# Optimization experiments

Hardware: AMD Instinct MI355X
Metric: run time of the kernel (lower is better)

Reference implementation:

```python
import jax, jax.numpy as jnp
import numpy as np

N = 100000
C_IN = 128
HEADS = 4
D_HEAD = 32
E = 1600000
NEG_SLOPE = 0.2
LN_EPS = 1e-5


def setup_inputs() -> dict:
    key = jax.random.key(0)
    ks = jax.random.split(key, 8)
    x = jax.random.normal(ks[0], (N, C_IN), dtype=jnp.float32)
    edge_index = jax.random.randint(ks[1], (2, E), 0, N, dtype=jnp.int32)
    # LayerNorm affine params
    ln_gamma = jnp.ones((C_IN,), jnp.float32)
    ln_beta = jnp.zeros((C_IN,), jnp.float32)
    # GATv2 linear layers (lin_l for source/messages, lin_r for target), glorot-ish scale
    scale = 1.0 / np.sqrt(C_IN)
    W_l = jax.random.normal(ks[2], (C_IN, HEADS * D_HEAD), jnp.float32) * scale
    b_l = jnp.zeros((HEADS * D_HEAD,), jnp.float32)
    W_r = jax.random.normal(ks[3], (C_IN, HEADS * D_HEAD), jnp.float32) * scale
    b_r = jnp.zeros((HEADS * D_HEAD,), jnp.float32)
    att = jax.random.normal(ks[4], (HEADS, D_HEAD), jnp.float32) * (1.0 / np.sqrt(D_HEAD))
    bias = jnp.zeros((D_HEAD,), jnp.float32)  # concat=False -> out_channels bias
    return {"x": x, "edge_index": edge_index, "ln_gamma": ln_gamma, "ln_beta": ln_beta,
            "W_l": W_l, "b_l": b_l, "W_r": W_r, "b_r": b_r, "att": att, "bias": bias}


def reference(x, edge_index, ln_gamma, ln_beta, W_l, b_l, W_r, b_r, att, bias):
    n = x.shape[0]
    # LayerNorm + ReLU (dropout_mask=None / eval mode)
    mu = jnp.mean(x, axis=-1, keepdims=True)
    var = jnp.mean(jnp.square(x - mu), axis=-1, keepdims=True)
    xh = (x - mu) * jax.lax.rsqrt(var + LN_EPS) * ln_gamma + ln_beta
    xh = jax.nn.relu(xh)
    # add self loops
    loops = jnp.arange(n, dtype=edge_index.dtype)
    src = jnp.concatenate([edge_index[0], loops])  # message sources j
    dst = jnp.concatenate([edge_index[1], loops])  # aggregation targets i
    # GATv2: separate transforms for source and target
    x_l = (xh @ W_l + b_l).reshape(n, HEADS, D_HEAD)
    x_r = (xh @ W_r + b_r).reshape(n, HEADS, D_HEAD)
    # edge scores: e_ij = att . leaky_relu(x_l[j] + x_r[i])
    s = x_l[src] + x_r[dst]                                      # [E+N, H, Dh]
    e = jnp.einsum('ehd,hd->eh', jax.nn.leaky_relu(s, NEG_SLOPE), att)
    # segment softmax over destination node
    m = jax.ops.segment_max(e, dst, num_segments=n)              # [N, H]
    w = jnp.exp(e - m[dst])
    denom = jax.ops.segment_sum(w, dst, num_segments=n)          # [N, H]
    alpha = w / (denom[dst] + 1e-16)                             # [E+N, H]
    # scatter-aggregate messages alpha * x_l[j]
    out = jax.ops.segment_sum(alpha[:, :, None] * x_l[src], dst, num_segments=n)  # [N, H, Dh]
    # concat=False -> mean over heads, then bias
    return out.mean(axis=1) + bias
```

## Files before the change

kernel.cpp:

```cpp
#include <hip/hip_runtime.h>
#include <math.h>


typedef __bf16 bf16x8 __attribute__((ext_vector_type(8)));
typedef float f32x4 __attribute__((ext_vector_type(4)));
typedef _Float16 h2 __attribute__((ext_vector_type(2)));

#define BIN_T 4096
#define NB_MAX 1024
#define AST 136
#define HST 136

static __device__ __forceinline__ unsigned short f2bf(float f) {
  union { float f; unsigned u; } v;
  v.f = f;
  const unsigned r = v.u + 0x7fffu + ((v.u >> 16) & 1u);
  return (unsigned short)(r >> 16);
}
static __device__ __forceinline__ float bf2f(unsigned short h) {
  union { float f; unsigned u; } v;
  v.u = ((unsigned)h) << 16;
  return v.f;
}

static __device__ __forceinline__ float quad_reduce_add(float p) {
  int a = __builtin_amdgcn_mov_dpp(__builtin_bit_cast(int, p),
                                   0xB1 , 0xf, 0xf,
                                   true);
  p += __builtin_bit_cast(float, a);
  int b = __builtin_amdgcn_mov_dpp(__builtin_bit_cast(int, p),
                                   0x4E , 0xf, 0xf,
                                   true);
  p += __builtin_bit_cast(float, b);
  return p;
}

__global__ __launch_bounds__(256) void hist_pack_k(
    const int* __restrict__ dst_arr, int* __restrict__ bucket_cnt,
    const float* __restrict__ Wl, const float* __restrict__ Wr,
    unsigned short* __restrict__ wph, unsigned short* __restrict__ wpl,
    int E, int NB) {
  __shared__ int h[NB_MAX];
  const int t = threadIdx.x;
  const int gtid = blockIdx.x * 256 + t;
  for (int b = t; b < NB; b += 256) h[b] = 0;
  if (gtid < 32768) {
    const int mat = gtid >> 14;
    const int rem = gtid & 16383;
    const int k = rem >> 7;
    const int c = rem & 127;
    const float v = (mat ? Wr : Wl)[rem];
    const unsigned short hh = f2bf(v);
    const unsigned short lo = f2bf(v - bf2f(hh));
    const int po = ((mat * 4 + (k >> 5)) * 128 + c) * 32 + (k & 31);
    wph[po] = hh;
    wpl[po] = lo;
  }
  __syncthreads();
  const int beg = blockIdx.x * BIN_T;
  const int end = min(beg + BIN_T, E);
  for (int j0 = beg + t * 4; j0 < end; j0 += 1024) {
    if (j0 + 4 <= end) {
      const int4 d4 = *(const int4*)(dst_arr + j0);
      atomicAdd(&h[d4.x >> 7], 1);
      atomicAdd(&h[d4.y >> 7], 1);
      atomicAdd(&h[d4.z >> 7], 1);
      atomicAdd(&h[d4.w >> 7], 1);
    } else {
      for (int j = j0; j < end; j++) atomicAdd(&h[dst_arr[j] >> 7], 1);
    }
  }
  __syncthreads();
  for (int b = t; b < NB; b += 256) {
    const int v = h[b];
    if (v) atomicAdd(&bucket_cnt[b], v);
  }
}

__global__ __launch_bounds__(1024) void bucket_scan_k(
    const int* __restrict__ bucket_cnt, int* __restrict__ bucket_edge_off,
    int* __restrict__ bucket_cur, int* __restrict__ offsets,
    int NB, int N, int M) {
  __shared__ int lds[1024];
  const int t = threadIdx.x;
  const int v = (t < NB) ? bucket_cnt[t] : 0;
  lds[t] = v;
  __syncthreads();
  for (int d = 1; d < 1024; d <<= 1) {
    int u = 0;
    if (t >= d) u = lds[t - d];
    __syncthreads();
    lds[t] += u;
    __syncthreads();
  }
  if (t < NB) {
    const int excl = lds[t] - v;
    bucket_edge_off[t] = excl;
    bucket_cur[t] = excl;
    if (t == NB - 1) bucket_edge_off[NB] = lds[t];
  }
  if (t == 0) offsets[N] = M;
}

__global__ __launch_bounds__(512, 5) void gemm_bin_fat_k(
    const float* __restrict__ x, const float* __restrict__ gamma,
    const float* __restrict__ beta,
    const unsigned short* __restrict__ wph,
    const unsigned short* __restrict__ wpl,
    const float* __restrict__ bl, const float* __restrict__ br,
    _Float16* __restrict__ xl16, _Float16* __restrict__ xr16,
    const int* __restrict__ ei, int* __restrict__ bucket_cur,
    unsigned* __restrict__ binned,
    int n, int E, int NB, int nchunks) {
  __shared__ char smem[64 * AST * 2 * 2];
  const int t = threadIdx.x;

  if ((int)blockIdx.x < nchunks) {
    int* const h = (int*)smem;
    int* const cur = h + NB_MAX;
    for (int b = t; b < NB; b += 512) h[b] = 0;
    __syncthreads();
    const int beg = blockIdx.x * BIN_T;
    const int end = min(beg + BIN_T, E);
    for (int j0 = beg + t * 4; j0 < end; j0 += 2048) {
      if (j0 + 4 <= end) {
        const int4 d4 = *(const int4*)(ei + E + j0);
        atomicAdd(&h[d4.x >> 7], 1);
        atomicAdd(&h[d4.y >> 7], 1);
        atomicAdd(&h[d4.z >> 7], 1);
        atomicAdd(&h[d4.w >> 7], 1);
      } else {
        for (int j = j0; j < end; j++) atomicAdd(&h[ei[E + j] >> 7], 1);
      }
    }
    __syncthreads();
    for (int b = t; b < NB; b += 512) {
      const int v = h[b];
      cur[b] = v ? atomicAdd(&bucket_cur[b], v) : 0;
    }
    __syncthreads();
    for (int j0 = beg + t * 4; j0 < end; j0 += 2048) {
      if (j0 + 4 <= end) {
        const int4 s4 = *(const int4*)(ei + j0);
        const int4 d4 = *(const int4*)(ei + E + j0);
        binned[atomicAdd(&cur[d4.x >> 7], 1)] =
            (((unsigned)d4.x & 127u) << 25) | (unsigned)s4.x;
        binned[atomicAdd(&cur[d4.y >> 7], 1)] =
            (((unsigned)d4.y & 127u) << 25) | (unsigned)s4.y;
        binned[atomicAdd(&cur[d4.z >> 7], 1)] =
            (((unsigned)d4.z & 127u) << 25) | (unsigned)s4.z;
        binned[atomicAdd(&cur[d4.w >> 7], 1)] =
            (((unsigned)d4.w & 127u) << 25) | (unsigned)s4.w;
      } else {
        for (int j = j0; j < end; j++) {
          const int s = ei[j], d = ei[E + j];
          binned[atomicAdd(&cur[d >> 7], 1)] =
              (((unsigned)d & 127u) << 25) | (unsigned)s;
        }
      }
    }
    return;
  }

  unsigned short* const ah = (unsigned short*)smem;
  unsigned short* const al = ah + 64 * AST;
  _Float16* const sth = (_Float16*)smem;
  const int blk = (blockIdx.x - nchunks) * 64;

  {
    const int r = t >> 3, q = t & 7;
    const int node = blk + r;
    float4 v[4];
    float s = 0.f, s2 = 0.f;
    const float* xrow = x + (size_t)node * 128;
#pragma unroll
    for (int rep = 0; rep < 4; rep++) {
      float4 f = make_float4(0.f, 0.f, 0.f, 0.f);
      if (node < n) f = *(const float4*)(xrow + 4 * q + 32 * rep);
      v[rep] = f;
      s += f.x + f.y + f.z + f.w;
      s2 += f.x * f.x + f.y * f.y + f.z * f.z + f.w * f.w;
    }
    s += __shfl_xor(s, 1);  s += __shfl_xor(s, 2);  s += __shfl_xor(s, 4);
    s2 += __shfl_xor(s2, 1); s2 += __shfl_xor(s2, 2); s2 += __shfl_xor(s2, 4);
    const float mu = s * (1.f / 128.f);
    const float rs = rsqrtf(s2 * (1.f / 128.f) - mu * mu + 1e-5f);
#pragma unroll
    for (int rep = 0; rep < 4; rep++) {
      const int k0 = 4 * q + 32 * rep;
      const float4 g4 = *(const float4*)(gamma + k0);
      const float4 b4 = *(const float4*)(beta + k0);
      const float ev[4] = {v[rep].x, v[rep].y, v[rep].z, v[rep].w};
      const float gv[4] = {g4.x, g4.y, g4.z, g4.w};
      const float bv[4] = {b4.x, b4.y, b4.z, b4.w};
      unsigned short hs[4], ls[4];
#pragma unroll
      for (int i2 = 0; i2 < 4; i2++) {
        float xv = (ev[i2] - mu) * rs * gv[i2] + bv[i2];
        xv = fmaxf(xv, 0.f);
        const unsigned short h = f2bf(xv);
        hs[i2] = h;
        ls[i2] = f2bf(xv - bf2f(h));
      }
      *(ushort4*)(&ah[r * AST + k0]) = make_ushort4(hs[0], hs[1], hs[2], hs[3]);
      *(ushort4*)(&al[r * AST + k0]) = make_ushort4(ls[0], ls[1], ls[2], ls[3]);
    }
  }
  __syncthreads();

  const int lane = t & 63;
  const int w = t >> 6;
  const int mat = w >> 2;
  const int cbase = (w & 3) * 32;
  const int m16 = lane & 15;
  const int quad = lane >> 4;
  const float* const biasp = mat ? br : bl;

  f32x4 acc[2][4];
  float bc[2];
#pragma unroll
  for (int ct = 0; ct < 2; ct++) {
    const int c = cbase + ct * 16 + m16;
    bf16x8 Bh[4], Bl8[4];
#pragma unroll
    for (int kb = 0; kb < 4; kb++) {
      const int bo = ((mat * 4 + kb) * 128 + c) * 32 + quad * 8;
      Bh[kb]  = *(const bf16x8*)(wph + bo);
      Bl8[kb] = *(const bf16x8*)(wpl + bo);
    }
    bc[ct] = biasp[c];
#pragma unroll
    for (int rt = 0; rt < 4; rt++) {
      f32x4 a = {0.f, 0.f, 0.f, 0.f};
#pragma unroll
      for (int kb = 0; kb < 4; kb++) {
        const int ao = (rt * 16 + m16) * AST + kb * 32 + quad * 8;
        const bf16x8 Ah  = *(const bf16x8*)(ah + ao);
        const bf16x8 Al8 = *(const bf16x8*)(al + ao);
        a = __builtin_amdgcn_mfma_f32_16x16x32_bf16(Ah,  Bh[kb],  a, 0, 0, 0);
        a = __builtin_amdgcn_mfma_f32_16x16x32_bf16(Al8, Bh[kb],  a, 0, 0, 0);
        a = __builtin_amdgcn_mfma_f32_16x16x32_bf16(Ah,  Bl8[kb], a, 0, 0, 0);
      }
      acc[ct][rt] = a;
    }
  }

  unsigned short* const outs[2] = {(unsigned short*)xl16,
                                   (unsigned short*)xr16};
#pragma unroll
  for (int round = 0; round < 2; round++) {
    __syncthreads();
    if (mat == 1 - round) {
#pragma unroll
      for (int ct = 0; ct < 2; ct++)
#pragma unroll
        for (int rt = 0; rt < 4; rt++)
#pragma unroll
          for (int g = 0; g < 4; g++)
            sth[(rt * 16 + quad * 4 + g) * HST + cbase + ct * 16 + m16] =
                (_Float16)(acc[ct][rt][g] + bc[ct]);
    }
    __syncthreads();
    unsigned short* const dst = outs[1 - round];
#pragma unroll
    for (int pass = 0; pass < 2; pass++) {
      const int idx = pass * 512 + t;
      const int row = idx >> 4;
      const int c8 = (idx & 15) * 8;
      const int node = blk + row;
      if (node < n)
        *(uint4*)(dst + (size_t)node * 128 + c8) =
            *(const uint4*)((const unsigned short*)sth + row * HST + c8);
    }
  }
}

__global__ __launch_bounds__(512) void csr_build_k(
    const unsigned* __restrict__ binned,
    const int* __restrict__ bucket_edge_off,
    unsigned* __restrict__ csr_src, int* __restrict__ offsets, int N, int M) {
  __shared__ int s_cnt[128];
  __shared__ int s_off[128];
  __shared__ int s_cur[128];
  const int b = blockIdx.x;
  const int t = threadIdx.x;
  if (b == 0 && t < 16) csr_src[M + t] = 0;
  const int eb = bucket_edge_off[b];
  const int ee = bucket_edge_off[b + 1];
  const int node0 = b << 7;
  if (t < 128) s_cnt[t] = 0;
  __syncthreads();
  for (int j = eb + t; j < ee; j += 512) {
    atomicAdd(&s_cnt[binned[j] >> 25], 1);
  }
  __syncthreads();
  int w = 0;
  if (t < 128) w = (node0 + t < N) ? (s_cnt[t] + 1) : 0;
  if (t < 128) s_off[t] = w;
  __syncthreads();
  for (int d = 1; d < 128; d <<= 1) {
    int u = 0;
    if (t < 128 && t >= d) u = s_off[t - d];
    __syncthreads();
    if (t < 128) s_off[t] += u;
    __syncthreads();
  }
  const int base = eb + node0;
  if (t < 128) {
    const int excl = s_off[t] - w;
    const int node = node0 + t;
    if (node < N) {
      offsets[node] = base + excl;
      csr_src[base + excl] = (unsigned)node << 8;
      s_cur[t] = excl + 1;
    }
  }
  __syncthreads();
  for (int j = eb + t; j < ee; j += 512) {
    const unsigned e = binned[j];
    const int pos = atomicAdd(&s_cur[e >> 25], 1);
    csr_src[base + pos] = (e & 0x1ffffffu) << 8;
  }
}

__global__ __launch_bounds__(256) void agg_fused_k(
    const uint4* __restrict__ xl4, const uint4* __restrict__ xr4,
    const float* __restrict__ att, const unsigned* __restrict__ csr_src,
    const int* __restrict__ offsets, const float* __restrict__ bias,
    float* __restrict__ out, int n) {
  const int t = threadIdx.x;
  const int wid = t >> 6;
  const int lane = t & 63;
  const int u = lane & 15;
  const int g = lane >> 4;
  const int nwaves = gridDim.x * 4;

  h2 at[4];
  {
    const float L2E = 1.44269504f;
    const float4 a0 = *(const float4*)(att + u * 8);
    const float4 a1 = *(const float4*)(att + u * 8 + 4);
    at[0] = h2{(_Float16)(a0.x * L2E), (_Float16)(a0.y * L2E)};
    at[1] = h2{(_Float16)(a0.z * L2E), (_Float16)(a0.w * L2E)};
    at[2] = h2{(_Float16)(a1.x * L2E), (_Float16)(a1.y * L2E)};
    at[3] = h2{(_Float16)(a1.z * L2E), (_Float16)(a1.w * L2E)};
  }
  float4 b0, b1;
  if (lane < 4) {
    b0 = *(const float4*)(bias + lane * 8);
    b1 = *(const float4*)(bias + lane * 8 + 4);
  }

  const h2 slope = h2{(_Float16)0.2f, (_Float16)0.2f};
  const char* const xbu = (const char*)xl4 + ((unsigned)u << 4);
  union U { uint4 u4; h2 h[4]; unsigned ui[4]; };

  int i = blockIdx.x * 4 + wid;
  if (i >= n) return;

  int off = offsets[i];
  int end = offsets[i + 1];
  U xru; xru.u4 = xr4[(size_t)i * 16 + u];
  uint4 rA = *(const uint4*)(xbu + csr_src[off + g]);
  uint4 rB = *(const uint4*)(xbu + csr_src[off + 4 + g]);

  while (true) {
    const int inext = i + nwaves;
    const int isel = (inext < n) ? inext : i;
    const int offn = offsets[isel];
    const int endn = offsets[isel + 1];
    U xrn; xrn.u4 = xr4[(size_t)isel * 16 + u];

    float den = 0.f;
    float acc[8] = {0.f, 0.f, 0.f, 0.f, 0.f, 0.f, 0.f, 0.f};

    for (int jb = off; jb < end; jb += 4) {
      U xv; xv.u4 = rA;
      rA = rB;
      rB = *(const uint4*)(xbu + csr_src[jb + 8 + g]);

      float p = 0.f;
#pragma unroll
      for (int k = 0; k < 4; k++) {
        const h2 s = xv.h[k] + xru.h[k];
        const h2 l = __builtin_elementwise_max(s, s * slope);
        p = __builtin_amdgcn_fdot2(l, at[k], p, false);
      }
      p = quad_reduce_add(p);

      const float wgt = (jb + g < end) ? __builtin_amdgcn_exp2f(p) : 0.f;
      den += wgt;
#pragma unroll
      for (int k = 0; k < 4; k++) {
        asm("v_fma_mix_f32 %0, %1, %2, %0 op_sel:[0,0,0] op_sel_hi:[0,1,0]"
            : "+v"(acc[2 * k]) : "v"(wgt), "v"(xv.ui[k]));
        asm("v_fma_mix_f32 %0, %1, %2, %0 op_sel:[0,1,0] op_sel_hi:[0,1,0]"
            : "+v"(acc[2 * k + 1]) : "v"(wgt), "v"(xv.ui[k]));
      }
    }

    const unsigned niA = csr_src[offn + g];
    const unsigned niB = csr_src[offn + 4 + g];

    den += __shfl_xor(den, 16);
    den += __shfl_xor(den, 32);
#pragma unroll
    for (int m = 0; m < 8; m++) {
      acc[m] += __shfl_xor(acc[m], 16);
      acc[m] += __shfl_xor(acc[m], 32);
    }
    const float rd = 1.0f / (den + 1e-16f);
#pragma unroll
    for (int m = 0; m < 8; m++) acc[m] *= rd;
#pragma unroll
    for (int m = 0; m < 8; m++) {
      acc[m] += __shfl_xor(acc[m], 4);
      acc[m] += __shfl_xor(acc[m], 8);
    }
    if (lane < 4) {
      float4 o0 = make_float4(acc[0] * 0.25f + b0.x, acc[1] * 0.25f + b0.y,
                              acc[2] * 0.25f + b0.z, acc[3] * 0.25f + b0.w);
      float4 o1 = make_float4(acc[4] * 0.25f + b1.x, acc[5] * 0.25f + b1.y,
                              acc[6] * 0.25f + b1.z, acc[7] * 0.25f + b1.w);
      *(float4*)(out + (size_t)i * 32 + lane * 8) = o0;
      *(float4*)(out + (size_t)i * 32 + lane * 8 + 4) = o1;
    }

    if (inext >= n) break;
    i = inext;
    off = offn;
    end = endn;
    xru = xrn;
    rA = *(const uint4*)(xbu + niA);
    rB = *(const uint4*)(xbu + niB);
  }
}

extern "C" void kernel_launch(void* const* d_in, const int* in_sizes, int n_in,
                              void* d_out, int out_size, void* d_ws,
                              size_t ws_size, hipStream_t stream) {
  const float* x     = (const float*)d_in[0];
  const int*   ei    = (const int*)d_in[1];
  const float* gamma = (const float*)d_in[2];
  const float* beta  = (const float*)d_in[3];
  const float* Wl    = (const float*)d_in[4];
  const float* bl    = (const float*)d_in[5];
  const float* Wr    = (const float*)d_in[6];
  const float* br    = (const float*)d_in[7];
  const float* att   = (const float*)d_in[8];
  const float* bias  = (const float*)d_in[9];
  float* out = (float*)d_out;

  const int N = in_sizes[0] / 128;
  const int E = in_sizes[1] / 2;
  const int M = E + N;
  const int NB = (N + 127) / 128;
  const int nchunks = (E + BIN_T - 1) / BIN_T;

  char* p = (char*)d_ws;
  size_t o = 0;
  auto alloc = [&](size_t bytes) -> void* {
    void* r = (void*)(p + o);
    o = (o + bytes + 255) & ~(size_t)255;
    return r;
  };
  _Float16* xl16 = (_Float16*)alloc((size_t)N * 128 * 2);
  _Float16* xr16 = (_Float16*)alloc((size_t)N * 128 * 2);
  unsigned* csr_src = (unsigned*)alloc((size_t)M * 4 + 64);
  int*   offsets = (int*)alloc((size_t)(N + 1) * 4);
  int*   bucket_cnt = (int*)alloc((size_t)NB * 4);
  int*   bucket_off = (int*)alloc((size_t)(NB + 1) * 4);
  int*   bucket_cur = (int*)alloc((size_t)NB * 4);
  unsigned short* wph = (unsigned short*)alloc(2 * 128 * 128 * 2);
  unsigned short* wpl = (unsigned short*)alloc(2 * 128 * 128 * 2);
  unsigned* binned = (unsigned*)out;
  (void)n_in; (void)out_size; (void)ws_size;

  hipMemsetAsync(bucket_cnt, 0, (size_t)NB * 4, stream);
  hist_pack_k<<<nchunks, 256, 0, stream>>>(ei + E, bucket_cnt, Wl, Wr, wph,
                                           wpl, E, NB);
  bucket_scan_k<<<1, 1024, 0, stream>>>(bucket_cnt, bucket_off, bucket_cur,
                                        offsets, NB, N, M);

  {
    const int gemmBlocks = (N + 63) / 64;
    gemm_bin_fat_k<<<nchunks + gemmBlocks, 512, 0, stream>>>(
        x, gamma, beta, wph, wpl, bl, br, xl16, xr16,
        ei, bucket_cur, binned, N, E, NB, nchunks);
  }

  csr_build_k<<<NB, 512, 0, stream>>>(binned, bucket_off, csr_src, offsets,
                                      N, M);

  const int nodeWaves = (N + 3) / 4;
  const int aggBlocks = nodeWaves < 2048 ? nodeWaves : 2048;
  agg_fused_k<<<aggBlocks, 256, 0, stream>>>((const uint4*)xl16,
                                             (const uint4*)xr16, att,
                                             csr_src, offsets, bias, out, N);
}
```

Measured before the change: 244.7 us.

## Store LDS A-tiles in MFMA fragment order and reorder GEMM loop over k

The normalized bf16 hi/lo activations are now written to shared memory in a fragment-contiguous layout that matches the MFMA operand pattern, in place of a padded row-major layout. The GEMM loop is restructured so k is outermost and each A fragment loaded from LDS is reused across both column tiles, which halves the LDS reads of A. Weight fragments are loaded per k step, which lowers their register footprint. The risk is more live accumulators and possible LDS bank conflicts on the fragment-order writes.

```diff
diff --git a/kernel.cpp b/kernel.cpp
--- a/kernel.cpp
+++ b/kernel.cpp
@@ -8,7 +8,6 @@
 
 #define BIN_T 4096
 #define NB_MAX 1024
-#define AST 136
 #define HST 136
 
 static __device__ __forceinline__ unsigned short f2bf(float f) {
@@ -112,7 +111,7 @@
     const int* __restrict__ ei, int* __restrict__ bucket_cur,
     unsigned* __restrict__ binned,
     int n, int E, int NB, int nchunks) {
-  __shared__ char smem[64 * AST * 2 * 2];
+  __shared__ char smem[34816];
   const int t = threadIdx.x;
 
   if ((int)blockIdx.x < nchunks) {
@@ -163,13 +162,17 @@
   }
 
   unsigned short* const ah = (unsigned short*)smem;
-  unsigned short* const al = ah + 64 * AST;
+  unsigned short* const al = ah + 8192;
   _Float16* const sth = (_Float16*)smem;
   const int blk = (blockIdx.x - nchunks) * 64;
 
   {
     const int r = t >> 3, q = t & 7;
     const int node = blk + r;
+    const int rt_r = r >> 4;
+    const int m16r = r & 15;
+    const int fq = q >> 1;
+    const int fo = (q & 1) * 4;
     float4 v[4];
     float s = 0.f, s2 = 0.f;
     const float* xrow = x + (size_t)node * 128;
@@ -202,8 +205,9 @@
         hs[i2] = h;
         ls[i2] = f2bf(xv - bf2f(h));
       }
-      *(ushort4*)(&ah[r * AST + k0]) = make_ushort4(hs[0], hs[1], hs[2], hs[3]);
-      *(ushort4*)(&al[r * AST + k0]) = make_ushort4(ls[0], ls[1], ls[2], ls[3]);
+      const int fidx = (((rt_r * 4 + rep) * 4 + fq) * 16 + m16r) * 8 + fo;
+      *(ushort4*)(&ah[fidx]) = make_ushort4(hs[0], hs[1], hs[2], hs[3]);
+      *(ushort4*)(&al[fidx]) = make_ushort4(ls[0], ls[1], ls[2], ls[3]);
     }
   }
   __syncthreads();
@@ -217,31 +221,38 @@
   const float* const biasp = mat ? br : bl;
 
   f32x4 acc[2][4];
+#pragma unroll
+  for (int ct = 0; ct < 2; ct++)
+#pragma unroll
+    for (int rt = 0; rt < 4; rt++)
+      acc[ct][rt] = f32x4{0.f, 0.f, 0.f, 0.f};
   float bc[2];
 #pragma unroll
-  for (int ct = 0; ct < 2; ct++) {
-    const int c = cbase + ct * 16 + m16;
-    bf16x8 Bh[4], Bl8[4];
-#pragma unroll
-    for (int kb = 0; kb < 4; kb++) {
+  for (int ct = 0; ct < 2; ct++) bc[ct] = biasp[cbase + ct * 16 + m16];
+
+#pragma unroll
+  for (int kb = 0; kb < 4; kb++) {
+    bf16x8 Bh[2], Bl8[2];
+#pragma unroll
+    for (int ct = 0; ct < 2; ct++) {
+      const int c = cbase + ct * 16 + m16;
       const int bo = ((mat * 4 + kb) * 128 + c) * 32 + quad * 8;
-      Bh[kb]  = *(const bf16x8*)(wph + bo);
-      Bl8[kb] = *(const bf16x8*)(wpl + bo);
-    }
-    bc[ct] = biasp[c];
+      Bh[ct]  = *(const bf16x8*)(wph + bo);
+      Bl8[ct] = *(const bf16x8*)(wpl + bo);
+    }
 #pragma unroll
     for (int rt = 0; rt < 4; rt++) {
-      f32x4 a = {0.f, 0.f, 0.f, 0.f};
-#pragma unroll
-      for (int kb = 0; kb < 4; kb++) {
-        const int ao = (rt * 16 + m16) * AST + kb * 32 + quad * 8;
-        const bf16x8 Ah  = *(const bf16x8*)(ah + ao);
-        const bf16x8 Al8 = *(const bf16x8*)(al + ao);
-        a = __builtin_amdgcn_mfma_f32_16x16x32_bf16(Ah,  Bh[kb],  a, 0, 0, 0);
-        a = __builtin_amdgcn_mfma_f32_16x16x32_bf16(Al8, Bh[kb],  a, 0, 0, 0);
-        a = __builtin_amdgcn_mfma_f32_16x16x32_bf16(Ah,  Bl8[kb], a, 0, 0, 0);
+      const int ao = (((rt * 4 + kb) * 4 + quad) * 16 + m16) * 8;
+      const bf16x8 Ah  = *(const bf16x8*)(ah + ao);
+      const bf16x8 Al8 = *(const bf16x8*)(al + ao);
+#pragma unroll
+      for (int ct = 0; ct < 2; ct++) {
+        f32x4 a = acc[ct][rt];
+        a = __builtin_amdgcn_mfma_f32_16x16x32_bf16(Ah,  Bh[ct],  a, 0, 0, 0);
+        a = __builtin_amdgcn_mfma_f32_16x16x32_bf16(Al8, Bh[ct],  a, 0, 0, 0);
+        a = __builtin_amdgcn_mfma_f32_16x16x32_bf16(Ah,  Bl8[ct], a, 0, 0, 0);
+        acc[ct][rt] = a;
       }
-      acc[ct][rt] = a;
     }
   }
 
```

Result: faster. 239.2 us (-2.3%).
